# Performance work log

Hardware: AMD Instinct MI355X
Metric: run time of the kernel (lower is better)

Reference implementation:

```python
import jax, jax.numpy as jnp
import numpy as np


def setup_inputs() -> dict:
    key = jax.random.key(0)
    k1, k2, k3, k4 = jax.random.split(key, 4)
    bs, ch, T = 8, 256, 512
    N, P = 2048, 16
    feat = jax.random.normal(k1, (bs, ch, T), dtype=jnp.float32)
    # rois: [N, 3] = (batch_idx, start, end) in feature coordinates
    bidx = jax.random.randint(k2, (N,), 0, bs).astype(jnp.float32)
    u1 = jax.random.uniform(k3, (N,), dtype=jnp.float32)
    u2 = jax.random.uniform(k4, (N,), dtype=jnp.float32)
    start = u1 * (T - 1)
    end = start + u2 * (T - start)
    rois = jnp.stack([bidx, start, end], axis=1).astype(jnp.float32)
    return {"input": feat, "rois": rois, "feature_dim": P, "ratio": 4}


def reference(input, rois, feature_dim, ratio):
    # 1D ROI Align: input [bs, ch, T], rois [N, 3]=(batch_idx, start, end)
    # -> output [N, ch, feature_dim]
    bs, ch, T = input.shape
    bidx = rois[:, 0].astype(jnp.int32)              # [N]
    start = rois[:, 1]
    end = rois[:, 2]
    roi_len = jnp.maximum(end - start, 1.0)          # malformed ROI guard
    bin_size = roi_len / feature_dim                 # [N]
    S = ratio                                        # samples per bin (static)
    p = jnp.arange(feature_dim, dtype=jnp.float32)   # bin index
    s = (jnp.arange(S, dtype=jnp.float32) + 0.5) / S # fractional offset in bin
    # sample coordinates x: [N, P, S]
    x = start[:, None, None] + (p[None, :, None] + s[None, None, :]) * bin_size[:, None, None]
    valid = (x >= -1.0) & (x <= T)                   # out-of-range samples -> 0
    xc = jnp.clip(x, 0.0, T - 1)
    x_low = jnp.floor(xc).astype(jnp.int32)
    x_high = jnp.minimum(x_low + 1, T - 1)
    lx = xc - x_low.astype(jnp.float32)              # linear interp weight
    b = bidx[:, None, None]                          # [N,1,1]
    v_low = input[b, :, x_low]                       # [N, P, S, ch]
    v_high = input[b, :, x_high]                     # [N, P, S, ch]
    val = v_low * (1.0 - lx[..., None]) + v_high * lx[..., None]
    val = jnp.where(valid[..., None], val, 0.0)
    out = val.mean(axis=2)                           # average over samples -> [N, P, ch]
    return jnp.transpose(out, (0, 2, 1))             # [N, ch, P]
```

## Files before the change

kernel.cpp:

```cpp
#include <hip/hip_runtime.h>


#define T_DIM 512
#define CH    256
#define P_DIM 16
#define S_RAT 4
#define CTILE 8
#define NCT   (CH / CTILE)
#define RSPLIT 8
#define MAXSL  256
#define TSTRIDE 517

__global__ __launch_bounds__(256) void roialign_lds_kernel(
    const float* __restrict__ feat,
    const float* __restrict__ rois,
    float* __restrict__ out,
    int N)
{
    __shared__ float tile[CTILE * TSTRIDE];
    __shared__ float s_start[MAXSL];
    __shared__ float s_end[MAXSL];
    __shared__ int   s_idx[MAXSL];
    __shared__ int   s_cnt;

    const int ct  = blockIdx.x;
    const int r   = blockIdx.y;
    const int b   = blockIdx.z;
    const int tid = threadIdx.x;

    if (tid == 0) s_cnt = 0;

    {
        const int c = tid >> 5;
        const int q = tid & 31;
        const float4* src = (const float4*)(feat + ((size_t)b * CH + ct * CTILE + c) * T_DIM);
        float* drow = &tile[c * TSTRIDE];
#pragma unroll
        for (int k = 0; k < 4; ++k) {
            float4 v = src[q + 32 * k];
            const int o = 4 * (q + 32 * k);
            drow[o + 0] = v.x; drow[o + 1] = v.y;
            drow[o + 2] = v.z; drow[o + 3] = v.w;
        }
    }
    __syncthreads();

    {
        const int i = r * MAXSL + tid;
        if (i < N) {
            float bf = rois[3 * i];
            if ((int)bf == b) {
                int pos = atomicAdd(&s_cnt, 1);
                s_idx[pos]   = i;
                s_start[pos] = rois[3 * i + 1];
                s_end[pos]   = rois[3 * i + 2];
            }
        }
    }
    __syncthreads();
    const int cnt = s_cnt;

    const int g    = tid >> 7;
    const int t128 = tid & 127;
    const int c    = t128 >> 4;
    const int p    = t128 & 15;
    const float* trow = &tile[c * TSTRIDE];
    const int c_out = (ct * CTILE + c) * P_DIM + p;

    float qf[S_RAT];
#pragma unroll
    for (int s = 0; s < S_RAT; ++s)
        qf[s] = (float)p + ((float)s + 0.5f) * (1.0f / S_RAT);

#pragma unroll 2
    for (int i = g; i < cnt; i += 2) {
        const float start = s_start[i];
        const float bin   = fmaxf(s_end[i] - start, 1.0f) * (1.0f / P_DIM);

        float acc = 0.0f;
#pragma unroll
        for (int s = 0; s < S_RAT; ++s) {
            float x  = fmaf(qf[s], bin, start);
            float xc = fminf(x, (float)(T_DIM - 1));
            float tf = fminf(truncf(xc), (float)(T_DIM - 2));
            int   t  = (int)tf;
            float wh = (xc - tf) * (1.0f / S_RAT);
            float wl = (1.0f / S_RAT) - wh;
            acc = fmaf(trow[t], wl, fmaf(trow[t + 1], wh, acc));
        }
        out[(size_t)s_idx[i] * (CH * P_DIM) + c_out] = acc;
    }
}

extern "C" void kernel_launch(void* const* d_in, const int* in_sizes, int n_in,
                              void* d_out, int out_size, void* d_ws, size_t ws_size,
                              hipStream_t stream) {
    const float* feat = (const float*)d_in[0];
    const float* rois = (const float*)d_in[1];
    float* out = (float*)d_out;
    const int N = in_sizes[1] / 3;

    dim3 grid(NCT, RSPLIT, 8);
    roialign_lds_kernel<<<grid, dim3(256), 0, stream>>>(feat, rois, out, N);
}
```

Measured before the change: 83.20 us.

## Pre-bin ROIs per batch in a separate kernel and balance work across splits

Adds a small pre-pass kernel that groups ROI indices and coordinates per batch into a workspace list. The main kernel then divides each batch's list evenly across its eight y-blocks, so every block no longer scans 256 rois with a shared-memory atomic filter and block sizes are balanced. Roi metadata is prefetched one iteration ahead from global memory. This costs an extra kernel launch with a serial dependency and adds a fallback path for when the workspace is too small.

Result: slower. 97.56 us (+17.3%).

```diff
diff --git a/kernel.cpp b/kernel.cpp
--- a/kernel.cpp
+++ b/kernel.cpp
@@ -7,28 +7,45 @@
 #define S_RAT 4
 #define CTILE 8
 #define NCT   (CH / CTILE)
-#define RSPLIT 8
-#define MAXSL  256
+#define JSPLIT 8
 #define TSTRIDE 517
+#define MAXN  2048
+#define NB    8
 
-__global__ __launch_bounds__(256) void roialign_lds_kernel(
+
+__global__ __launch_bounds__(256) void bin_rois_kernel(
+    const float* __restrict__ rois, int N,
+    int* __restrict__ cnt, float4* __restrict__ lists)
+{
+    __shared__ int s_cnt;
+    const int b   = blockIdx.x;
+    const int tid = threadIdx.x;
+    if (tid == 0) s_cnt = 0;
+    __syncthreads();
+    for (int i = tid; i < N; i += 256) {
+        float bf = rois[3 * i];
+        if ((int)bf == b) {
+            int pos = atomicAdd(&s_cnt, 1);
+            lists[b * MAXN + pos] =
+                make_float4((float)i, rois[3 * i + 1], rois[3 * i + 2], 0.0f);
+        }
+    }
+    __syncthreads();
+    if (tid == 0) cnt[b] = s_cnt;
+}
+
+__global__ __launch_bounds__(256) void roialign_main_kernel(
     const float* __restrict__ feat,
-    const float* __restrict__ rois,
-    float* __restrict__ out,
-    int N)
+    const int*   __restrict__ cnt,
+    const float4* __restrict__ lists,
+    float* __restrict__ out)
 {
     __shared__ float tile[CTILE * TSTRIDE];
-    __shared__ float s_start[MAXSL];
-    __shared__ float s_end[MAXSL];
-    __shared__ int   s_idx[MAXSL];
-    __shared__ int   s_cnt;
 
     const int ct  = blockIdx.x;
-    const int r   = blockIdx.y;
+    const int j   = blockIdx.y;
     const int b   = blockIdx.z;
     const int tid = threadIdx.x;
-
-    if (tid == 0) s_cnt = 0;
 
     {
         const int c = tid >> 5;
@@ -43,22 +60,11 @@
             drow[o + 2] = v.z; drow[o + 3] = v.w;
         }
     }
-    __syncthreads();
 
-    {
-        const int i = r * MAXSL + tid;
-        if (i < N) {
-            float bf = rois[3 * i];
-            if ((int)bf == b) {
-                int pos = atomicAdd(&s_cnt, 1);
-                s_idx[pos]   = i;
-                s_start[pos] = rois[3 * i + 1];
-                s_end[pos]   = rois[3 * i + 2];
-            }
-        }
-    }
-    __syncthreads();
-    const int cnt = s_cnt;
+    const int cb    = cnt[b];
+    const int share = (cb + JSPLIT - 1) / JSPLIT;
+    const int lo    = j * share;
+    const int hi    = min(lo + share, cb);
 
     const int g    = tid >> 7;
     const int t128 = tid & 127;
@@ -72,10 +78,16 @@
     for (int s = 0; s < S_RAT; ++s)
         qf[s] = (float)p + ((float)s + 0.5f) * (1.0f / S_RAT);
 
-#pragma unroll 2
-    for (int i = g; i < cnt; i += 2) {
-        const float start = s_start[i];
-        const float bin   = fmaxf(s_end[i] - start, 1.0f) * (1.0f / P_DIM);
+    __syncthreads();
+
+    const float4* mylist = lists + b * MAXN;
+    int i = lo + g;
+    float4 meta = (i < hi) ? mylist[i] : make_float4(0.f, 0.f, 0.f, 0.f);
+    for (; i < hi; i += 2) {
+        float4 next = (i + 2 < hi) ? mylist[i + 2] : meta;
+
+        const float start = meta.y;
+        const float bin   = fmaxf(meta.z - start, 1.0f) * (1.0f / P_DIM);
 
         float acc = 0.0f;
 #pragma unroll
@@ -86,6 +98,59 @@
             int   t  = (int)tf;
             float wh = (xc - tf) * (1.0f / S_RAT);
             float wl = (1.0f / S_RAT) - wh;
+            float va = trow[t];
+            float vb = trow[t + 1];
+            acc = fmaf(va, wl, fmaf(vb, wh, acc));
+        }
+        out[(size_t)(int)meta.x * (CH * P_DIM) + c_out] = acc;
+        meta = next;
+    }
+}
+
+__global__ __launch_bounds__(256) void roialign_fallback_kernel(
+    const float* __restrict__ feat, const float* __restrict__ rois,
+    float* __restrict__ out, int N)
+{
+    __shared__ float tile[CTILE * TSTRIDE];
+    __shared__ float s_start[256], s_end[256];
+    __shared__ int   s_idx[256], s_cnt;
+    const int ct = blockIdx.x, r = blockIdx.y, b = blockIdx.z, tid = threadIdx.x;
+    if (tid == 0) s_cnt = 0;
+    {
+        const int c = tid >> 5, q = tid & 31;
+        const float4* src = (const float4*)(feat + ((size_t)b * CH + ct * CTILE + c) * T_DIM);
+        float* drow = &tile[c * TSTRIDE];
+#pragma unroll
+        for (int k = 0; k < 4; ++k) {
+            float4 v = src[q + 32 * k];
+            const int o = 4 * (q + 32 * k);
+            drow[o] = v.x; drow[o + 1] = v.y; drow[o + 2] = v.z; drow[o + 3] = v.w;
+        }
+    }
+    __syncthreads();
+    {
+        const int i = r * 256 + tid;
+        if (i < N && (int)rois[3 * i] == b) {
+            int pos = atomicAdd(&s_cnt, 1);
+            s_idx[pos] = i; s_start[pos] = rois[3 * i + 1]; s_end[pos] = rois[3 * i + 2];
+        }
+    }
+    __syncthreads();
+    const int cnt = s_cnt;
+    const int g = tid >> 7, t128 = tid & 127, c = t128 >> 4, p = t128 & 15;
+    const float* trow = &tile[c * TSTRIDE];
+    const int c_out = (ct * CTILE + c) * P_DIM + p;
+    for (int i = g; i < cnt; i += 2) {
+        const float start = s_start[i];
+        const float bin = fmaxf(s_end[i] - start, 1.0f) * (1.0f / P_DIM);
+        float acc = 0.0f;
+#pragma unroll
+        for (int s = 0; s < S_RAT; ++s) {
+            float x  = fmaf((float)p + ((float)s + 0.5f) * 0.25f, bin, start);
+            float xc = fminf(x, 511.0f);
+            float tf = fminf(truncf(xc), 510.0f);
+            int   t  = (int)tf;
+            float wh = (xc - tf) * 0.25f, wl = 0.25f - wh;
             acc = fmaf(trow[t], wl, fmaf(trow[t + 1], wh, acc));
         }
         out[(size_t)s_idx[i] * (CH * P_DIM) + c_out] = acc;
@@ -100,6 +165,13 @@
     float* out = (float*)d_out;
     const int N = in_sizes[1] / 3;
 
-    dim3 grid(NCT, RSPLIT, 8);
-    roialign_lds_kernel<<<grid, dim3(256), 0, stream>>>(feat, rois, out, N);
+    const size_t need = 256 + (size_t)NB * MAXN * sizeof(float4);
+    if (ws_size >= need && N <= MAXN) {
+        int*    cnt   = (int*)d_ws;
+        float4* lists = (float4*)((char*)d_ws + 256);
+        bin_rois_kernel<<<dim3(NB), dim3(256), 0, stream>>>(rois, N, cnt, lists);
+        roialign_main_kernel<<<dim3(NCT, JSPLIT, NB), dim3(256), 0, stream>>>(feat, cnt, lists, out);
+    } else {
+        roialign_fallback_kernel<<<dim3(NCT, 8, NB), dim3(256), 0, stream>>>(feat, rois, out, N);
+    }
 }
```
